# Optimization experiments

Measured on AMD Instinct MI355X. Metric: run time of the kernel, lower is better.

## Reference

```python
import jax, jax.numpy as jnp
import numpy as np


def _conv(x, w, b, pad):
    y = jax.lax.conv_general_dilated(x, w, (1, 1), [(pad, pad), (pad, pad)],
                                     dimension_numbers=('NCHW', 'OIHW', 'NCHW'))
    return y + b[None, :, None, None]


def _group_norm(x, gamma, beta, groups=4, eps=1e-5):
    B, C, H, W = x.shape
    xg = x.reshape(B, groups, C // groups, H, W)
    mu = xg.mean(axis=(2, 3, 4), keepdims=True)
    var = ((xg - mu) ** 2).mean(axis=(2, 3, 4), keepdims=True)
    xn = ((xg - mu) * jax.lax.rsqrt(var + eps)).reshape(B, C, H, W)
    return xn * gamma[None, :, None, None] + beta[None, :, None, None]


def _deform_conv2d(x, offsets, weight, bias, pad=1):
    # torchvision-style deform_conv2d, stride=1, dilation=1, 1 offset group.
    # x: [B,C,H,W]; offsets: [B,2*9,H,W] interleaved (dy,dx) per 3x3 tap (row-major).
    B, C, H, W = x.shape
    K = 9
    off = offsets.reshape(B, K, 2, H, W)
    ki = jnp.arange(3)
    gi = jnp.repeat(ki, 3).astype(x.dtype)  # kernel row index per tap
    gj = jnp.tile(ki, 3).astype(x.dtype)    # kernel col index per tap
    # sampling position: p = p_out + (k - pad) + offset
    py = off[:, :, 0] + jnp.arange(H, dtype=x.dtype)[None, None, :, None] + (gi - pad)[None, :, None, None]
    px = off[:, :, 1] + jnp.arange(W, dtype=x.dtype)[None, None, None, :] + (gj - pad)[None, :, None, None]
    y0 = jnp.floor(py)
    x0 = jnp.floor(px)
    wy1 = py - y0  # [B,K,H,W]
    wx1 = px - x0
    xf = x.reshape(B, C, H * W)

    def gather(yi, xi):
        valid = (yi >= 0) & (yi < H) & (xi >= 0) & (xi < W)
        yc = jnp.clip(yi, 0, H - 1).astype(jnp.int32)
        xc = jnp.clip(xi, 0, W - 1).astype(jnp.int32)
        idx = (yc * W + xc).reshape(B, 1, K * H * W)
        v = jnp.take_along_axis(xf, idx, axis=2).reshape(B, C, K, H, W)
        return v * valid.astype(x.dtype)[:, None]  # zero-pad outside

    sampled = (gather(y0, x0) * ((1 - wy1) * (1 - wx1))[:, None]
               + gather(y0, x0 + 1) * ((1 - wy1) * wx1)[:, None]
               + gather(y0 + 1, x0) * (wy1 * (1 - wx1))[:, None]
               + gather(y0 + 1, x0 + 1) * (wy1 * wx1)[:, None])  # [B,C,K,H,W]
    out = jnp.einsum('bckhw,ock->bohw', sampled, weight.reshape(weight.shape[0], C, K))
    return out + bias[None, :, None, None]


def setup_inputs() -> dict:
    key = jax.random.key(0)
    ks = jax.random.split(key, 8)
    B, C, H, W = 8, 256, 128, 128
    mid = max(C // 4, 32)  # 64
    f32 = jnp.float32
    return {
        "features": jax.random.normal(ks[0], (B, C, H, W), f32),
        "wind_uv": jax.random.normal(ks[1], (B, 2, H, W), f32),
        "compress_w": jax.random.normal(ks[2], (mid, C, 1, 1), f32) * 0.05,
        "compress_b": jnp.zeros((mid,), f32),
        "off1_w": jax.random.normal(ks[3], (32, 2, 3, 3), f32) * 0.1,
        "off1_b": jnp.zeros((32,), f32),
        "off2_w": jax.random.normal(ks[4], (18, 32, 3, 3), f32) * 0.05,
        "off2_b": jnp.zeros((18,), f32),
        "deform_w": jax.random.normal(ks[5], (mid, mid, 3, 3), f32) * 0.02,
        "deform_b": jnp.zeros((mid,), f32),
        "expand_w": jax.random.normal(ks[6], (C, mid, 1, 1), f32) * 0.05,
        "expand_b": jnp.zeros((C,), f32),
        "gn_gamma": jnp.ones((C,), f32),
        "gn_beta": jnp.zeros((C,), f32),
    }


def reference(features, wind_uv, compress_w, compress_b, off1_w, off1_b,
              off2_w, off2_b, deform_w, deform_b, expand_w, expand_b,
              gn_gamma, gn_beta):
    x = _conv(features, compress_w, compress_b, 0)
    h = jax.nn.gelu(_conv(wind_uv, off1_w, off1_b, 1), approximate=False)
    offsets = _conv(h, off2_w, off2_b, 1)
    x = _deform_conv2d(x, offsets, deform_w, deform_b, pad=1)
    x = _conv(x, expand_w, expand_b, 0)
    return features + jax.nn.gelu(_group_norm(x, gn_gamma, gn_beta), approximate=False)
```

## Files before the change

### kernel.cpp

```cpp
#include <hip/hip_runtime.h>
#include <math.h>


#define BB 8
#define CC 256
#define HW 16384
#define MID 64

typedef __attribute__((ext_vector_type(8))) short bf16x8;
typedef __attribute__((ext_vector_type(4))) float f32x4;

__device__ __forceinline__ float gelu_f(float v){
  return 0.5f*v*(1.0f + erff(v*0.7071067811865476f));
}
__device__ __forceinline__ unsigned f2bf(float f){
  union { float f; unsigned u; } v; v.f = f;
  unsigned u = v.u;
  u += 0x7fff + ((u >> 16) & 1);
  return (u >> 16);
}

__global__ void k_prep(const float* __restrict__ dw, const float* __restrict__ cw,
                       const float* __restrict__ ew, ushort* __restrict__ bt,
                       ushort* __restrict__ cwb, ushort* __restrict__ ewb){
  int i = blockIdx.x*256 + threadIdx.x;
  if (i < 36864){
    int k = i >> 12, r = i & 4095;
    int o = r >> 6, c = r & 63;
    bt[i] = (ushort)f2bf(dw[(o*64+c)*9 + k]);
  }
  int j = i - 36864;
  if (j >= 0 && j < 16384) cwb[j] = (ushort)f2bf(cw[j]);
  int l = i - 53248;
  if (l >= 0 && l < 16384) ewb[l] = (ushort)f2bf(ew[l]);
}

__global__ __launch_bounds__(256) void k_compress(const float* __restrict__ feat,
    const ushort* __restrict__ cwb, const float* __restrict__ cb, float* __restrict__ xo){
  __shared__ ushort A[128*64];
  int t = threadIdx.x;
  int b = blockIdx.y, p0 = blockIdx.x*128;
  int lane = t & 63, w = t >> 6, ln = lane & 15, qd = lane >> 4;
  int n = (w<<4) + ln;
  int cg = t >> 4, pxg = t & 15;
  f32x4 acc[8];
  #pragma unroll
  for (int pt=0;pt<8;pt++) acc[pt] = (f32x4){0.f,0.f,0.f,0.f};
  for (int kt=0;kt<4;kt++){
    const float* fb = feat + ((size_t)(b*CC + kt*64 + cg*4))*HW + p0 + pxg*8;
    float v[4][8];
    #pragma unroll
    for (int i=0;i<4;i++){
      *(float4*)&v[i][0] = *(const float4*)(fb + (size_t)i*HW);
      *(float4*)&v[i][4] = *(const float4*)(fb + (size_t)i*HW + 4);
    }
    __syncthreads();
    #pragma unroll
    for (int j=0;j<8;j++){
      int px = pxg*8 + j;
      unsigned lo = f2bf(v[0][j]) | (f2bf(v[1][j])<<16);
      unsigned hi = f2bf(v[2][j]) | (f2bf(v[3][j])<<16);
      int chunk = (cg>>1) ^ (px&7);
      *(uint2*)((char*)A + px*128 + chunk*16 + (cg&1)*8) = make_uint2(lo,hi);
    }
    __syncthreads();
    const ushort* wb = cwb + (size_t)n*256 + kt*64 + (qd<<3);
    bf16x8 b0 = *(const bf16x8*)wb;
    bf16x8 b1 = *(const bf16x8*)(wb + 32);
    #pragma unroll
    for (int pt=0;pt<8;pt++){
      int m = (pt<<4) + ln;
      int ch0 = qd ^ (m&7), ch1 = (4+qd) ^ (m&7);
      bf16x8 a0 = *(bf16x8*)(A + (m<<6) + (ch0<<3));
      acc[pt] = __builtin_amdgcn_mfma_f32_16x16x32_bf16(a0, b0, acc[pt], 0,0,0);
      bf16x8 a1 = *(bf16x8*)(A + (m<<6) + (ch1<<3));
      acc[pt] = __builtin_amdgcn_mfma_f32_16x16x32_bf16(a1, b1, acc[pt], 0,0,0);
    }
  }
  float bias = cb[n];
  float* xp = xo + ((size_t)(b*HW + p0))*64 + n;
  #pragma unroll
  for (int pt=0;pt<8;pt++){
    #pragma unroll
    for (int rg=0;rg<4;rg++){
      int px = (pt<<4) + (qd<<2) + rg;
      xp[(size_t)px*64] = acc[pt][rg] + bias;
    }
  }
}

__global__ __launch_bounds__(256) void k_off1(const float* __restrict__ wind,
    const float* __restrict__ w1, const float* __restrict__ b1, float* __restrict__ ho){
  __shared__ float wl[576];
  int t=threadIdx.x;
  for (int i=t;i<576;i+=256) wl[i]=w1[i];
  __syncthreads();
  int b=blockIdx.y; int p=blockIdx.x*256+t;
  int y=p>>7, x=p&127;
  float tap[18];
  #pragma unroll
  for (int c=0;c<2;c++){
    #pragma unroll
    for (int ki=0;ki<3;ki++){
      #pragma unroll
      for (int kj=0;kj<3;kj++){
        int yy=y+ki-1, xx=x+kj-1;
        float v=0.f;
        if ((unsigned)yy<128u && (unsigned)xx<128u)
          v = wind[((size_t)b*2+c)*HW + (yy<<7)+xx];
        tap[c*9+ki*3+kj]=v;
      }
    }
  }
  float outv[32];
  #pragma unroll
  for (int o=0;o<32;o++){
    float a=b1[o];
    #pragma unroll
    for (int i=0;i<18;i++) a += tap[i]*wl[o*18+i];
    outv[o]=gelu_f(a);
  }
  float* hp = ho + ((size_t)(b*HW+p))*32;
  #pragma unroll
  for (int o=0;o<32;o+=4) *(float4*)(hp+o)=make_float4(outv[o],outv[o+1],outv[o+2],outv[o+3]);
}

__global__ __launch_bounds__(256) void k_off2(const float* __restrict__ h,
    const float* __restrict__ w2, const float* __restrict__ b2, float* __restrict__ oo){
  __shared__ float wl[9*18*32];
  int t=threadIdx.x;
  for (int i=t;i<5184;i+=256){
    int k=i/576; int r=i-k*576; int o=r>>5; int c=r&31;
    wl[i] = w2[(o*32+c)*9+k];
  }
  __syncthreads();
  int b=blockIdx.y; int p=blockIdx.x*256+t;
  int y=p>>7, x=p&127;
  float acc[18];
  #pragma unroll
  for (int o=0;o<18;o++) acc[o]=b2[o];
  for (int ki=0;ki<3;ki++){
    for (int kj=0;kj<3;kj++){
      int k = ki*3+kj;
      int yy=y+ki-1, xx=x+kj-1;
      float4 hv[8];
      if ((unsigned)yy<128u && (unsigned)xx<128u){
        const float* hp = h + ((size_t)(b*HW) + (yy<<7)+xx)*32;
        #pragma unroll
        for (int q=0;q<8;q++) hv[q]=*(const float4*)(hp+q*4);
      } else {
        #pragma unroll
        for (int q=0;q<8;q++) hv[q]=make_float4(0.f,0.f,0.f,0.f);
      }
      const float* wk = &wl[k*576];
      #pragma unroll
      for (int o=0;o<18;o++){
        float a=acc[o];
        #pragma unroll
        for (int q=0;q<8;q++){
          float4 w4 = *(const float4*)(wk + o*32 + q*4);
          a += hv[q].x*w4.x + hv[q].y*w4.y + hv[q].z*w4.z + hv[q].w*w4.w;
        }
        acc[o]=a;
      }
    }
  }
  float* op = oo + ((size_t)(b*HW+p))*18;
  #pragma unroll
  for (int o=0;o<18;o+=2) *(float2*)(op+o)=make_float2(acc[o],acc[o+1]);
}

__global__ __launch_bounds__(256) void k_deform(
    const float* __restrict__ x, const float* __restrict__ off,
    const ushort* __restrict__ bt, const float* __restrict__ db,
    float* __restrict__ yo){
  __shared__ ushort A[128*64];
  __shared__ float offs[128*18];
  int t = threadIdx.x;
  int blk = blockIdx.x;
  int b = blk & 7, r = blk >> 3;
  int p0 = r*128;
  const float* offg = off + ((size_t)(b*HW + p0))*18;
  for (int i=t;i<576;i+=256)
    *(float4*)(offs + i*4) = *(const float4*)(offg + i*4);
  __syncthreads();
  int lane = t & 63, w = t >> 6, ln = lane & 15, qd = lane >> 4;
  int n = (w<<4) + ln;
  const float* xb = x + (size_t)b*HW*64;
  f32x4 acc[8];
  #pragma unroll
  for (int pt=0;pt<8;pt++) acc[pt] = (f32x4){0.f,0.f,0.f,0.f};

  for (int k=0;k<9;k++){
    int ki = k/3, kj = k - ki*3;
    const ushort* btk = bt + (size_t)(((k<<6) + n)<<6) + (qd<<3);
    bf16x8 bf0 = *(const bf16x8*)btk;
    bf16x8 bf1 = *(const bf16x8*)(btk + 32);
    __syncthreads();
    #pragma unroll
    for (int pp=0;pp<8;pp++){
      int p = (w<<5) + (pp<<2) + qd;
      float2 dd = *(const float2*)(offs + p*18 + 2*k);
      float py  = dd.x + (float)(r + ki - 1);
      float pxs = dd.y + (float)(p + kj - 1);
      float y0f = floorf(py), x0f = floorf(pxs);
      float fy = py - y0f, fx = pxs - x0f;
      int y0 = (int)y0f, x0 = (int)x0f;
      float w00=(1.f-fy)*(1.f-fx), w01=(1.f-fy)*fx, w10=fy*(1.f-fx), w11=fy*fx;
      bool v0=((unsigned)y0<128u), v1=((unsigned)(y0+1)<128u);
      bool u0=((unsigned)x0<128u), u1=((unsigned)(x0+1)<128u);
      w00 = (v0&&u0)? w00 : 0.f;  w01 = (v0&&u1)? w01 : 0.f;
      w10 = (v1&&u0)? w10 : 0.f;  w11 = (v1&&u1)? w11 : 0.f;
      int y0c = min(max(y0,0),127), y1c = min(max(y0+1,0),127);
      int x0c = min(max(x0,0),127), x1c = min(max(x0+1,0),127);
      int cofs = (ln<<2);
      const float4* r00 = (const float4*)(xb + (size_t)y0c*8192 + x0c*64 + cofs);
      const float4* r01 = (const float4*)(xb + (size_t)y0c*8192 + x1c*64 + cofs);
      const float4* r10 = (const float4*)(xb + (size_t)y1c*8192 + x0c*64 + cofs);
      const float4* r11 = (const float4*)(xb + (size_t)y1c*8192 + x1c*64 + cofs);
      float4 a00=*r00, a01=*r01, a10=*r10, a11=*r11;
      float4 s;
      s.x = a00.x*w00 + a01.x*w01 + a10.x*w10 + a11.x*w11;
      s.y = a00.y*w00 + a01.y*w01 + a10.y*w10 + a11.y*w11;
      s.z = a00.z*w00 + a01.z*w01 + a10.z*w10 + a11.z*w11;
      s.w = a00.w*w00 + a01.w*w01 + a10.w*w10 + a11.w*w11;
      unsigned lo = f2bf(s.x) | (f2bf(s.y)<<16);
      unsigned hi = f2bf(s.z) | (f2bf(s.w)<<16);
      int chunk = (ln>>1) ^ (p&7);
      *(uint2*)((char*)A + p*128 + chunk*16 + (ln&1)*8) = make_uint2(lo,hi);
    }
    __syncthreads();
    #pragma unroll
    for (int pt=0;pt<8;pt++){
      int m = (pt<<4) + ln;
      int ch0 = qd ^ (m&7), ch1 = (4+qd) ^ (m&7);
      bf16x8 a0 = *(bf16x8*)(A + (m<<6) + (ch0<<3));
      acc[pt] = __builtin_amdgcn_mfma_f32_16x16x32_bf16(a0, bf0, acc[pt], 0,0,0);
      bf16x8 a1 = *(bf16x8*)(A + (m<<6) + (ch1<<3));
      acc[pt] = __builtin_amdgcn_mfma_f32_16x16x32_bf16(a1, bf1, acc[pt], 0,0,0);
    }
  }
  float bias = db[n];
  float* yp = yo + ((size_t)(b*HW + p0))*64 + n;
  #pragma unroll
  for (int pt=0;pt<8;pt++){
    #pragma unroll
    for (int rg=0;rg<4;rg++){
      int px = (pt<<4) + (qd<<2) + rg;
      yp[(size_t)px*64] = acc[pt][rg] + bias;
    }
  }
}

__global__ __launch_bounds__(256) void k_stats(const float* __restrict__ y,
    float* __restrict__ partY2, float* __restrict__ partYb){
  __shared__ float yt[128*64];
  int t=threadIdx.x; int b=blockIdx.y; int r=blockIdx.x;
  const float* yp = y + ((size_t)(b*HW) + (size_t)r*128)*64;
  for (int i=t*4;i<8192;i+=1024) *(float4*)&yt[i]=*(const float4*)(yp+i);
  __syncthreads();
  int ib = t & 15, jb = t >> 4;
  float acc[4][4];
  #pragma unroll
  for (int a=0;a<4;a++)
    #pragma unroll
    for (int c=0;c<4;c++) acc[a][c]=0.f;
  for (int p=0;p<128;p++){
    float4 vi = *(const float4*)&yt[(p<<6)+(ib<<2)];
    float4 vj = *(const float4*)&yt[(p<<6)+(jb<<2)];
    float fi[4]={vi.x,vi.y,vi.z,vi.w};
    float fj[4]={vj.x,vj.y,vj.z,vj.w};
    #pragma unroll
    for (int a=0;a<4;a++)
      #pragma unroll
      for (int c=0;c<4;c++) acc[a][c] += fi[a]*fj[c];
  }
  float* pb = partY2 + ((size_t)(b*128+r))*4096;
  #pragma unroll
  for (int a=0;a<4;a++)
    *(float4*)(pb + (ib*4+a)*64 + jb*4) =
        make_float4(acc[a][0],acc[a][1],acc[a][2],acc[a][3]);
  if (t < 64){
    float s=0.f;
    for (int p=0;p<128;p++) s += yt[(p<<6)+t];
    partYb[(size_t)(b*128+r)*64 + t] = s;
  }
}

__global__ __launch_bounds__(256) void k_reduce(const float* __restrict__ partY2,
    const float* __restrict__ partYb, float* __restrict__ Y2,
    float* __restrict__ ybar){
  int t=threadIdx.x; int b=blockIdx.y;
  if (blockIdx.x < 4){
    int e = (blockIdx.x*256 + t)*4;
    const float* p = partY2 + ((size_t)b*128)*4096 + e;
    float4 s=make_float4(0.f,0.f,0.f,0.f);
    for (int r=0;r<128;r++){
      float4 v=*(const float4*)(p+(size_t)r*4096);
      s.x+=v.x; s.y+=v.y; s.z+=v.z; s.w+=v.w;
    }
    *(float4*)(Y2+((size_t)b<<12)+e)=s;
  } else if (t < 16){
    int e = t*4;
    const float* p = partYb + (size_t)b*8192 + e;
    float4 s=make_float4(0.f,0.f,0.f,0.f);
    for (int r=0;r<128;r++){
      float4 v=*(const float4*)(p+r*64);
      s.x+=v.x; s.y+=v.y; s.z+=v.z; s.w+=v.w;
    }
    *(float4*)(ybar+(b<<6)+e)=s;
  }
}

__global__ __launch_bounds__(256) void k_gn(const float* __restrict__ Y2,
    const float* __restrict__ ybar, const float* __restrict__ ew,
    const float* __restrict__ eb, float* __restrict__ stats){
  __shared__ float wsm[64*65];
  __shared__ float red[512];
  int t=threadIdx.x;
  int bg=blockIdx.x, b=bg>>2, g=bg&3;
  for (int i=t;i<4096;i+=256){
    int c=i>>6, m=i&63;
    wsm[c*65+m] = ew[(((size_t)g<<6)+c)*64 + m];
  }
  __syncthreads();
  int c = t&63, qm = t>>6;
  const float* wv = &wsm[c*65];
  const float* Y2b = Y2 + ((size_t)b<<12);
  const float* yb = ybar + (b<<6);
  float q=0.f, sbp=0.f;
  for (int m=qm*16; m<qm*16+16; m++){
    const float* row = Y2b + (m<<6);
    float ym=0.f;
    for (int nn=0;nn<64;nn+=4){
      float4 r4=*(const float4*)(row+nn);
      ym += r4.x*wv[nn] + r4.y*wv[nn+1] + r4.z*wv[nn+2] + r4.w*wv[nn+3];
    }
    q += ym*wv[m];
    sbp += wv[m]*yb[m];
  }
  float bias = eb[(g<<6)+c];
  float pz  = sbp + (qm==0 ? 16384.f*bias : 0.f);
  float pz2 = q + 2.f*bias*sbp + (qm==0 ? 16384.f*bias*bias : 0.f);
  red[t]=pz; red[256+t]=pz2;
  __syncthreads();
  for (int s=128;s>0;s>>=1){
    if (t<s){ red[t]+=red[t+s]; red[256+t]+=red[256+t+s]; }
    __syncthreads();
  }
  if (t==0){
    const float N=64.f*16384.f;
    float mu = red[0]/N;
    float var = red[256]/N - mu*mu;
    stats[bg*2]=mu; stats[bg*2+1]=rsqrtf(var+1e-5f);
  }
}

__global__ __launch_bounds__(256) void k_final(const float* __restrict__ y,
    const ushort* __restrict__ ewb, const float* __restrict__ eb,
    const float* __restrict__ stats, const float* __restrict__ gamma,
    const float* __restrict__ beta, const float* __restrict__ feat,
    float* __restrict__ out){
  __shared__ ushort A[128*64];
  int t = threadIdx.x;
  int b = blockIdx.y, p0 = blockIdx.x*128;
  int lane = t & 63, w = t >> 6, ln = lane & 15, qd = lane >> 4;
  {
    int px = t>>1, ch0 = (t&1)*32;
    const float* yp = y + ((size_t)(b*HW + p0 + px))*64 + ch0;
    #pragma unroll
    for (int q=0;q<4;q++){
      float4 va = *(const float4*)(yp + q*8);
      float4 vb = *(const float4*)(yp + q*8 + 4);
      unsigned u0 = f2bf(va.x)|(f2bf(va.y)<<16);
      unsigned u1 = f2bf(va.z)|(f2bf(va.w)<<16);
      unsigned u2 = f2bf(vb.x)|(f2bf(vb.y)<<16);
      unsigned u3 = f2bf(vb.z)|(f2bf(vb.w)<<16);
      int chunk16 = (ch0 + q*8) >> 3;
      int phys = chunk16 ^ (px&7);
      *(uint4*)((char*)A + px*128 + phys*16) = make_uint4(u0,u1,u2,u3);
    }
  }
  __syncthreads();
  float mu = stats[((b<<2)+w)*2], rstd = stats[((b<<2)+w)*2+1];
  const float* fb = feat + (size_t)b*CC*HW + p0;
  float* ob = out + (size_t)b*CC*HW + p0;
  for (int nt=0;nt<4;nt++){
    int nch = (w<<6) + (nt<<4) + ln;
    const ushort* wb = ewb + (size_t)nch*64 + (qd<<3);
    bf16x8 b0 = *(const bf16x8*)wb;
    bf16x8 b1 = *(const bf16x8*)(wb + 32);
    f32x4 acc[8];
    #pragma unroll
    for (int pt=0;pt<8;pt++) acc[pt] = (f32x4){0.f,0.f,0.f,0.f};
    #pragma unroll
    for (int pt=0;pt<8;pt++){
      int m = (pt<<4) + ln;
      int ch0 = qd ^ (m&7), ch1 = (4+qd) ^ (m&7);
      bf16x8 a0 = *(bf16x8*)(A + (m<<6) + (ch0<<3));
      acc[pt] = __builtin_amdgcn_mfma_f32_16x16x32_bf16(a0, b0, acc[pt], 0,0,0);
      bf16x8 a1 = *(bf16x8*)(A + (m<<6) + (ch1<<3));
      acc[pt] = __builtin_amdgcn_mfma_f32_16x16x32_bf16(a1, b1, acc[pt], 0,0,0);
    }
    float bias = eb[nch];
    float ga = gamma[nch], be = beta[nch];
    float gr = rstd*ga;
    float ofs = (bias - mu)*gr + be;
    const float* frow = fb + (size_t)nch*HW;
    float* orow = ob + (size_t)nch*HW;
    #pragma unroll
    for (int pt=0;pt<8;pt++){
      int px = (pt<<4) + (qd<<2);
      float4 f = *(const float4*)(frow + px);
      float4 o;
      o.x = f.x + gelu_f(acc[pt][0]*gr + ofs);
      o.y = f.y + gelu_f(acc[pt][1]*gr + ofs);
      o.z = f.z + gelu_f(acc[pt][2]*gr + ofs);
      o.w = f.w + gelu_f(acc[pt][3]*gr + ofs);
      *(float4*)(orow + px) = o;
    }
  }
}

extern "C" void kernel_launch(void* const* d_in, const int* in_sizes, int n_in,
                              void* d_out, int out_size, void* d_ws, size_t ws_size,
                              hipStream_t stream){
  const float* feat = (const float*)d_in[0];
  const float* wind = (const float*)d_in[1];
  const float* cw   = (const float*)d_in[2];
  const float* cb   = (const float*)d_in[3];
  const float* w1   = (const float*)d_in[4];
  const float* b1   = (const float*)d_in[5];
  const float* w2   = (const float*)d_in[6];
  const float* b2   = (const float*)d_in[7];
  const float* dw   = (const float*)d_in[8];
  const float* db   = (const float*)d_in[9];
  const float* ew   = (const float*)d_in[10];
  const float* ebias= (const float*)d_in[11];
  const float* gg   = (const float*)d_in[12];
  const float* gb   = (const float*)d_in[13];
  float* ws = (float*)d_ws;
  float* x_nhwc   = ws;
  float* y_nhwc   = ws + 8388608;
  float* h_nhwc   = ws + 16777216;
  float* off_nhwc = ws + 20971520;
  ushort* bt      = (ushort*)(ws + 23330816);
  ushort* cwb     = (ushort*)(ws + 23349248);
  ushort* ewb     = (ushort*)(ws + 23357440);
  float* Y2       = ws + 23365632;
  float* ybar     = ws + 23398400;
  float* stats    = ws + 23398912;
  float* partY2   = h_nhwc;
  float* partYb   = off_nhwc;
  k_prep<<<272,256,0,stream>>>(dw, cw, ew, bt, cwb, ewb);
  k_compress<<<dim3(128,8),256,0,stream>>>(feat, cwb, cb, x_nhwc);
  k_off1<<<dim3(64,8),256,0,stream>>>(wind, w1, b1, h_nhwc);
  k_off2<<<dim3(64,8),256,0,stream>>>(h_nhwc, w2, b2, off_nhwc);
  k_deform<<<1024,256,0,stream>>>(x_nhwc, off_nhwc, bt, db, y_nhwc);
  k_stats<<<dim3(128,8),256,0,stream>>>(y_nhwc, partY2, partYb);
  k_reduce<<<dim3(5,8),256,0,stream>>>(partY2, partYb, Y2, ybar);
  k_gn<<<32,256,0,stream>>>(Y2, ybar, ew, ebias, stats);
  k_final<<<dim3(128,8),256,0,stream>>>(y_nhwc, ewb, ebias, stats, gg, gb, feat, (float*)d_out);
}
```

Measured before the change: 520.1 us.

## Store deform output as bf16 and halve k_final pixel tile

The deform conv output is now converted to bf16 inside k_deform, staged through shared memory, and written with coalesced 16-byte stores in place of strided fp32 scalar stores. k_stats and k_final read the bf16 intermediate, which halves that tensor's traffic, and k_final no longer needs its own fp32-to-bf16 conversion. k_final also moves to 64-pixel tiles with twice as many blocks. GroupNorm statistics are now computed from bf16-rounded values, so they are slightly less accurate than before.

```diff
diff --git a/kernel.cpp b/kernel.cpp
--- a/kernel.cpp
+++ b/kernel.cpp
@@ -18,6 +18,9 @@
   unsigned u = v.u;
   u += 0x7fff + ((u >> 16) & 1);
   return (u >> 16);
+}
+__device__ __forceinline__ float bf2f(unsigned u){
+  union { unsigned u; float f; } v; v.u = u; return v.f;
 }
 
 __global__ void k_prep(const float* __restrict__ dw, const float* __restrict__ cw,
@@ -173,7 +176,7 @@
 __global__ __launch_bounds__(256) void k_deform(
     const float* __restrict__ x, const float* __restrict__ off,
     const ushort* __restrict__ bt, const float* __restrict__ db,
-    float* __restrict__ yo){
+    ushort* __restrict__ yo){
   __shared__ ushort A[128*64];
   __shared__ float offs[128*18];
   int t = threadIdx.x;
@@ -240,24 +243,38 @@
       acc[pt] = __builtin_amdgcn_mfma_f32_16x16x32_bf16(a1, bf1, acc[pt], 0,0,0);
     }
   }
+  __syncthreads();
   float bias = db[n];
-  float* yp = yo + ((size_t)(b*HW + p0))*64 + n;
   #pragma unroll
   for (int pt=0;pt<8;pt++){
     #pragma unroll
     for (int rg=0;rg<4;rg++){
       int px = (pt<<4) + (qd<<2) + rg;
-      yp[(size_t)px*64] = acc[pt][rg] + bias;
-    }
-  }
-}
-
-__global__ __launch_bounds__(256) void k_stats(const float* __restrict__ y,
+      A[(px<<6) + n] = (ushort)f2bf(acc[pt][rg] + bias);
+    }
+  }
+  __syncthreads();
+  uint4* yq = (uint4*)(yo + ((size_t)(b*HW + p0))*64);
+  const uint4* As = (const uint4*)A;
+  #pragma unroll
+  for (int q=0;q<4;q++) yq[t + q*256] = As[t + q*256];
+}
+
+__global__ __launch_bounds__(256) void k_stats(const ushort* __restrict__ y,
     float* __restrict__ partY2, float* __restrict__ partYb){
   __shared__ float yt[128*64];
   int t=threadIdx.x; int b=blockIdx.y; int r=blockIdx.x;
-  const float* yp = y + ((size_t)(b*HW) + (size_t)r*128)*64;
-  for (int i=t*4;i<8192;i+=1024) *(float4*)&yt[i]=*(const float4*)(yp+i);
+  const ushort* yp = y + ((size_t)(b*HW) + (size_t)r*128)*64;
+  for (int i=t*8;i<8192;i+=2048){
+    uint4 v = *(const uint4*)(yp+i);
+    float4 f0, f1;
+    f0.x = bf2f(v.x<<16); f0.y = bf2f(v.x&0xffff0000u);
+    f0.z = bf2f(v.y<<16); f0.w = bf2f(v.y&0xffff0000u);
+    f1.x = bf2f(v.z<<16); f1.y = bf2f(v.z&0xffff0000u);
+    f1.z = bf2f(v.w<<16); f1.w = bf2f(v.w&0xffff0000u);
+    *(float4*)&yt[i] = f0;
+    *(float4*)&yt[i+4] = f1;
+  }
   __syncthreads();
   int ib = t & 15, jb = t >> 4;
   float acc[4][4];
@@ -356,30 +373,23 @@
   }
 }
 
-__global__ __launch_bounds__(256) void k_final(const float* __restrict__ y,
+__global__ __launch_bounds__(256) void k_final(const ushort* __restrict__ y,
     const ushort* __restrict__ ewb, const float* __restrict__ eb,
     const float* __restrict__ stats, const float* __restrict__ gamma,
     const float* __restrict__ beta, const float* __restrict__ feat,
     float* __restrict__ out){
-  __shared__ ushort A[128*64];
+  __shared__ ushort A[64*64];
   int t = threadIdx.x;
-  int b = blockIdx.y, p0 = blockIdx.x*128;
+  int b = blockIdx.y, p0 = blockIdx.x*64;
   int lane = t & 63, w = t >> 6, ln = lane & 15, qd = lane >> 4;
   {
-    int px = t>>1, ch0 = (t&1)*32;
-    const float* yp = y + ((size_t)(b*HW + p0 + px))*64 + ch0;
-    #pragma unroll
-    for (int q=0;q<4;q++){
-      float4 va = *(const float4*)(yp + q*8);
-      float4 vb = *(const float4*)(yp + q*8 + 4);
-      unsigned u0 = f2bf(va.x)|(f2bf(va.y)<<16);
-      unsigned u1 = f2bf(va.z)|(f2bf(va.w)<<16);
-      unsigned u2 = f2bf(vb.x)|(f2bf(vb.y)<<16);
-      unsigned u3 = f2bf(vb.z)|(f2bf(vb.w)<<16);
-      int chunk16 = (ch0 + q*8) >> 3;
-      int phys = chunk16 ^ (px&7);
-      *(uint4*)((char*)A + px*128 + phys*16) = make_uint4(u0,u1,u2,u3);
-    }
+    int px = t>>2, ch0 = (t&3)*16;
+    const uint4* yp = (const uint4*)(y + ((size_t)(b*HW + p0 + px))*64 + ch0);
+    uint4 v0 = yp[0], v1 = yp[1];
+    int c16 = ch0 >> 3;
+    char* Ab = (char*)A + px*128;
+    *(uint4*)(Ab + ((c16  )^(px&7))*16) = v0;
+    *(uint4*)(Ab + ((c16+1)^(px&7))*16) = v1;
   }
   __syncthreads();
   float mu = stats[((b<<2)+w)*2], rstd = stats[((b<<2)+w)*2+1];
@@ -390,11 +400,11 @@
     const ushort* wb = ewb + (size_t)nch*64 + (qd<<3);
     bf16x8 b0 = *(const bf16x8*)wb;
     bf16x8 b1 = *(const bf16x8*)(wb + 32);
-    f32x4 acc[8];
-    #pragma unroll
-    for (int pt=0;pt<8;pt++) acc[pt] = (f32x4){0.f,0.f,0.f,0.f};
-    #pragma unroll
-    for (int pt=0;pt<8;pt++){
+    f32x4 acc[4];
+    #pragma unroll
+    for (int pt=0;pt<4;pt++) acc[pt] = (f32x4){0.f,0.f,0.f,0.f};
+    #pragma unroll
+    for (int pt=0;pt<4;pt++){
       int m = (pt<<4) + ln;
       int ch0 = qd ^ (m&7), ch1 = (4+qd) ^ (m&7);
       bf16x8 a0 = *(bf16x8*)(A + (m<<6) + (ch0<<3));
@@ -409,7 +419,7 @@
     const float* frow = fb + (size_t)nch*HW;
     float* orow = ob + (size_t)nch*HW;
     #pragma unroll
-    for (int pt=0;pt<8;pt++){
+    for (int pt=0;pt<4;pt++){
       int px = (pt<<4) + (qd<<2);
       float4 f = *(const float4*)(frow + px);
       float4 o;
@@ -441,7 +451,7 @@
   const float* gb   = (const float*)d_in[13];
   float* ws = (float*)d_ws;
   float* x_nhwc   = ws;
-  float* y_nhwc   = ws + 8388608;
+  ushort* y_bf16  = (ushort*)(ws + 8388608);
   float* h_nhwc   = ws + 16777216;
   float* off_nhwc = ws + 20971520;
   ushort* bt      = (ushort*)(ws + 23330816);
@@ -456,9 +466,9 @@
   k_compress<<<dim3(128,8),256,0,stream>>>(feat, cwb, cb, x_nhwc);
   k_off1<<<dim3(64,8),256,0,stream>>>(wind, w1, b1, h_nhwc);
   k_off2<<<dim3(64,8),256,0,stream>>>(h_nhwc, w2, b2, off_nhwc);
-  k_deform<<<1024,256,0,stream>>>(x_nhwc, off_nhwc, bt, db, y_nhwc);
-  k_stats<<<dim3(128,8),256,0,stream>>>(y_nhwc, partY2, partYb);
+  k_deform<<<1024,256,0,stream>>>(x_nhwc, off_nhwc, bt, db, y_bf16);
+  k_stats<<<dim3(128,8),256,0,stream>>>(y_bf16, partY2, partYb);
   k_reduce<<<dim3(5,8),256,0,stream>>>(partY2, partYb, Y2, ybar);
   k_gn<<<32,256,0,stream>>>(Y2, ybar, ew, ebias, stats);
-  k_final<<<dim3(128,8),256,0,stream>>>(y_nhwc, ewb, ebias, stats, gg, gb, feat, (float*)d_out);
-}
+  k_final<<<dim3(256,8),256,0,stream>>>(y_bf16, ewb, ebias, stats, gg, gb, feat, (float*)d_out);
+}
```

Result: faster. 509.1 us (-2.1%).
